# Optimization experiments

Measured on AMD Instinct MI355X. Metric: run time of the kernel, lower is better.

Reference implementation:

```python
import jax, jax.numpy as jnp
import numpy as np
import math

N, E, G = 16000, 128000, 64
D, H, O, L, HID = 64, 4, 64, 5, 128
EPS = 1e-5

def _ln(x, g, b):
    mu = x.mean(-1, keepdims=True)
    var = ((x - mu) ** 2).mean(-1, keepdims=True)
    return (x - mu) / jnp.sqrt(var + EPS) * g + b

def _softplus_b64(x):
    # torch nn.Softplus(beta=64, threshold=64): x if 64*x > 64 else log1p(exp(64*x))/64
    z = jnp.minimum(x * 64.0, 64.0)
    return jnp.where(x * 64.0 > 64.0, x, jnp.log1p(jnp.exp(z)) / 64.0)

def setup_inputs() -> dict:
    key = jax.random.key(0)
    ks = jax.random.split(key, 32)
    s = 0.05
    d = {
        'x': jax.random.normal(ks[0], (N, 4), jnp.float32),
        'edge_attr': jax.random.normal(ks[1], (E, 9), jnp.float32),
        'edge_index': jax.random.randint(ks[2], (2, E), 0, N),
        'batch': jnp.sort(jax.random.randint(ks[3], (N,), 0, G)),
        'W_atom': jax.random.normal(ks[4], (4, D)) * s, 'b_atom': jnp.zeros((D,)),
        'We1': jax.random.normal(ks[5], (9, D)) * s, 'be1': jnp.zeros((D,)),
        'We2': jax.random.normal(ks[6], (D, D)) * s, 'be2': jnp.zeros((D,)),
        'Wq': jax.random.normal(ks[7], (L, D, H * O)) * s, 'bq': jnp.zeros((L, H * O)),
        'Wk': jax.random.normal(ks[8], (L, D, H * O)) * s, 'bk': jnp.zeros((L, H * O)),
        'Wv': jax.random.normal(ks[9], (L, D, H * O)) * s, 'bv': jnp.zeros((L, H * O)),
        'Wedge': jax.random.normal(ks[10], (L, D, H * O)) * s, 'bedge': jnp.zeros((L, H * O)),
        'Wfea': jax.random.normal(ks[11], (L, D, O)) * s, 'bfea': jnp.zeros((L, O)),
        'Wcat': jax.random.normal(ks[12], (L, H * O, O)) * s, 'bcat': jnp.zeros((L, O)),
        'Wupd': jax.random.normal(ks[13], (L, 3 * O, 3 * O)) * s, 'bupd': jnp.zeros((L, 3 * O)),
        'Wmsg': jax.random.normal(ks[14], (L, 3 * O, O)) * s, 'bmsg': jnp.zeros((L, O)),
        'g_msg': jnp.ones((L, O)), 'be_msg': jnp.zeros((L, O)),
        'g_ln': jnp.ones((L, 3 * O)), 'be_ln': jnp.zeros((L, 3 * O)),
        'g_bn': jnp.ones((L, O)), 'be_bn': jnp.zeros((L, O)),
        'Wfc': jax.random.normal(ks[15], (D, HID)) * s, 'bfc': jnp.zeros((HID,)),
        'Wout': jax.random.normal(ks[16], (HID, 1)) * s, 'bout': jnp.zeros((1,)),
    }
    return d

def _forward(x, edge_attr, W_atom, b_atom, We1, be1, We2, be2, Wq, bq, Wk, bk, Wv, bv,
             Wedge, bedge, Wfea, bfea, Wcat, bcat, Wupd, bupd, Wmsg, bmsg,
             g_msg, be_msg, g_ln, be_ln, g_bn, be_bn, Wfc, bfc, Wout, bout,
             edge_index, batch):
    src, dst = edge_index[0], edge_index[1]  # x_j = src, x_i = dst (flow source_to_target)
    h = x @ W_atom + b_atom  # [N, D]
    e = _softplus_b64(edge_attr @ We1 + be1) @ We2 + be2  # [E, D]
    scale = 1.0 / math.sqrt(3.0 * O)
    for l in range(L):
        Q = (h @ Wq[l] + bq[l]).reshape(N, H, O)
        K = (h @ Wk[l] + bk[l]).reshape(N, H, O)
        V = (h @ Wv[l] + bv[l]).reshape(N, H, O)
        Eh = (e @ Wedge[l] + bedge[l]).reshape(E, H, O)
        Qi = Q[dst]
        q_ij = jnp.concatenate([Qi, Qi, Qi], axis=-1)                 # [E, H, 3O]
        k_ij = jnp.concatenate([K[dst], K[src], Eh], axis=-1)
        v_ij = jnp.concatenate([V[dst], V[src], Eh], axis=-1)
        alpha = q_ij * k_ij * scale
        gate = jax.nn.sigmoid(_ln(alpha, g_ln[l], be_ln[l]))
        m = gate * (v_ij @ Wupd[l] + bupd[l])
        m = _ln(m @ Wmsg[l] + bmsg[l], g_msg[l], be_msg[l])           # [E, H, O]
        agg = jax.ops.segment_sum(m, dst, num_segments=N).reshape(N, H * O)
        out = agg @ Wcat[l] + bcat[l]
        mu = out.mean(0)
        var = ((out - mu) ** 2).mean(0)  # biased var, BN training mode
        out = (out - mu) / jnp.sqrt(var + EPS) * g_bn[l] + be_bn[l]
        h = jax.nn.silu(out) + (h @ Wfea[l] + bfea[l])
    ones = jnp.ones((N,), h.dtype)
    cnt = jax.ops.segment_sum(ones, batch, num_segments=G)
    pooled = jax.ops.segment_sum(h, batch, num_segments=G) / jnp.maximum(cnt, 1.0)[:, None]
    z = jax.nn.silu(pooled @ Wfc + bfc)
    return z @ Wout + bout  # [G, 1]

def reference(x, edge_attr, edge_index, batch, W_atom, b_atom, We1, be1, We2, be2,
              Wq, bq, Wk, bk, Wv, bv, Wedge, bedge, Wfea, bfea, Wcat, bcat,
              Wupd, bupd, Wmsg, bmsg, g_msg, be_msg, g_ln, be_ln, g_bn, be_bn,
              Wfc, bfc, Wout, bout):
    return _forward(x, edge_attr, W_atom, b_atom, We1, be1, We2, be2, Wq, bq, Wk, bk,
                    Wv, bv, Wedge, bedge, Wfea, bfea, Wcat, bcat, Wupd, bupd,
                    Wmsg, bmsg, g_msg, be_msg, g_ln, be_ln, g_bn, be_bn,
                    Wfc, bfc, Wout, bout, edge_index, batch)
```

## Files before the change

kernel.cpp:

```cpp
#include <hip/hip_runtime.h>
#include <hip/hip_bf16.h>
#include <math.h>

#define N_NODES 16000
#define N_EDGES 128000
#define N_GRAPH 64
#define NL 5
#define EPSV 1e-5f
#define SCALE 0.07216878364870323f

#define PC 2048
#define ECOLS 1024
#define TILE 16
#define SCR 260

typedef __hip_bfloat16 bf16;
typedef __attribute__((ext_vector_type(8))) short short8;
typedef __attribute__((ext_vector_type(4))) short s4v;
typedef __attribute__((ext_vector_type(4))) float f32x4;
union S8U { short8 v; s4v h[2]; };

__device__ __forceinline__ ushort f2b(float x) {
    union { float f; uint u; } v; v.f = x;
    uint r = v.u + 0x7fffu + ((v.u >> 16) & 1u);
    return (ushort)(r >> 16);
}
__device__ __forceinline__ float b2fu(ushort u) { union { uint u; float f; } v; v.u = (uint)u << 16; return v.f; }

__global__ void pack_w(const float* __restrict__ Wq, const float* __restrict__ Wk,
                       const float* __restrict__ Wv, const float* __restrict__ Wupd,
                       const float* __restrict__ Wedge,
                       short* __restrict__ Wnp, short* __restrict__ Wep) {
    int idx = blockIdx.x * 256 + threadIdx.x;
    int total = NL * 64 * (PC + ECOLS);
    if (idx >= total) return;
    int c = idx % (PC + ECOLS);
    int k = (idx / (PC + ECOLS)) % 64;
    int l = idx / (64 * (PC + ECOLS));
    if (c < PC) {
        float v = 0.f;
        if (c < 256) v = Wq[(l*64 + k)*256 + c];
        else if (c < 512) v = Wk[(l*64 + k)*256 + (c - 256)];
        else if (c < 1280) {
            int cc = c - 512, hd = cc / 192, p = cc % 192;
            float s = 0.f;
            for (int q = 0; q < 64; ++q)
                s += Wv[(l*64 + k)*256 + hd*64 + q] * Wupd[(l*192 + q)*192 + p];
            v = s;
        } else {
            int cc = c - 1280, hd = cc / 192, p = cc % 192;
            float s = 0.f;
            for (int q = 0; q < 64; ++q)
                s += Wv[(l*64 + k)*256 + hd*64 + q] * Wupd[(l*192 + 64 + q)*192 + p];
            v = s;
        }
        int t = c >> 4, s = k >> 5, lane = (c & 15) | (((k & 31) >> 3) << 4), jj = k & 7;
        size_t fo = ((size_t)(t*2 + s)*64 + lane)*8 + jj;
        ushort hi = f2b(v);
        ushort lo = f2b(v - b2fu(hi));
        Wnp[(size_t)l*2*64*PC + fo] = (short)hi;
        Wnp[(size_t)l*2*64*PC + (size_t)64*PC + fo] = (short)lo;
    } else {
        int ce = c - PC;
        float v;
        if (ce < 256) v = Wedge[(l*64 + k)*256 + ce];
        else {
            int cc = ce - 256, hd = cc / 192, p = cc % 192;
            float s = 0.f;
            for (int q = 0; q < 64; ++q)
                s += Wedge[(l*64 + k)*256 + hd*64 + q] * Wupd[(l*192 + 128 + q)*192 + p];
            v = s;
        }
        int t = ce >> 4, s = k >> 5, lane = (ce & 15) | (((k & 31) >> 3) << 4), jj = k & 7;
        size_t fo = ((size_t)(t*2 + s)*64 + lane)*8 + jj;
        ushort hi = f2b(v);
        ushort lo = f2b(v - b2fu(hi));
        Wep[(size_t)l*2*64*ECOLS + fo] = (short)hi;
        Wep[(size_t)l*2*64*ECOLS + (size_t)64*ECOLS + fo] = (short)lo;
    }
}

__global__ void pack_wmsg(const float* __restrict__ Wmsg, short* __restrict__ Wmf) {
    int idx = blockIdx.x * 256 + threadIdx.x;
    if (idx >= NL*192*64) return;
    int col = idx & 63, k = (idx >> 6) % 192, l = idx / (192*64);
    float v = Wmsg[(size_t)(l*192 + k)*64 + col];
    int t = col >> 4, s = k >> 5, lane = (col & 15) | (((k & 31) >> 3) << 4), j = k & 7;
    Wmf[(size_t)l*12288 + ((size_t)((t*6 + s)*64) + lane)*8 + j] = (short)f2b(v);
}

__global__ void pack_b(const float* __restrict__ bq, const float* __restrict__ bk,
                       const float* __restrict__ bv, const float* __restrict__ Wupd,
                       const float* __restrict__ bupd, const float* __restrict__ bedge,
                       float* __restrict__ bnp, float* __restrict__ bep) {
    int idx = blockIdx.x * 256 + threadIdx.x;
    int total = NL * (PC + ECOLS);
    if (idx >= total) return;
    int c = idx % (PC + ECOLS);
    int l = idx / (PC + ECOLS);
    if (c < PC) {
        float v = 0.f;
        if (c < 256) v = bq[l*256 + c];
        else if (c < 512) v = bk[l*256 + c - 256];
        else if (c < 1280) {
            int cc = c - 512, hd = cc / 192, p = cc % 192;
            float s = 0.f;
            for (int k = 0; k < 64; ++k) s += bv[l*256 + hd*64 + k] * Wupd[(l*192 + k)*192 + p];
            v = s;
        } else {
            int cc = c - 1280, hd = cc / 192, p = cc % 192;
            float s = 0.f;
            for (int k = 0; k < 64; ++k) s += bv[l*256 + hd*64 + k] * Wupd[(l*192 + 64 + k)*192 + p];
            v = s;
        }
        bnp[l*PC + c] = v;
    } else {
        int ce = c - PC;
        float v;
        if (ce < 256) v = bedge[l*256 + ce];
        else {
            int cc = ce - 256, hd = cc / 192, p = cc % 192;
            float s = bupd[l*192 + p];
            for (int k = 0; k < 64; ++k) s += bedge[l*256 + hd*64 + k] * Wupd[(l*192 + 128 + k)*192 + p];
            v = s;
        }
        bep[l*ECOLS + ce] = v;
    }
}

__global__ void init_h(const float* __restrict__ x, const float* __restrict__ W_atom,
                       const float* __restrict__ b_atom, float* __restrict__ h) {
    int idx = blockIdx.x * 256 + threadIdx.x;
    int d = idx & 63, n = idx >> 6;
    float s = b_atom[d];
    #pragma unroll
    for (int j = 0; j < 4; ++j) s += x[n*4 + j] * W_atom[j*64 + d];
    h[idx] = s;
}

__global__ void init_e(const float* __restrict__ ea, const float* __restrict__ We1,
                       const float* __restrict__ be1, const float* __restrict__ We2,
                       const float* __restrict__ be2, float* __restrict__ ef) {
    __shared__ float sT[4][64];
    int tid = threadIdx.x, d = tid & 63, sub = tid >> 6;
    int e = blockIdx.x * 4 + sub;
    float s = be1[d];
    #pragma unroll
    for (int j = 0; j < 9; ++j) s += ea[e*9 + j] * We1[j*64 + d];
    float x64 = s * 64.f;
    float sp = (x64 > 64.f) ? s : log1pf(__expf(fminf(x64, 64.f))) * (1.f/64.f);
    sT[sub][d] = sp;
    float acc = be2[d];
    #pragma unroll
    for (int k = 0; k < 64; ++k) acc += sT[sub][k] * We2[k*64 + d];
    ef[(size_t)e*64 + d] = acc;
}

#define CPAD 260
__global__ __launch_bounds__(256, 8) void proj_mfma(
    const float* __restrict__ A, const short* __restrict__ Whi, const short* __restrict__ Wlo,
    const float* __restrict__ bias, ushort* __restrict__ out, int M) {
    __shared__ short aHi[2*64*8];
    __shared__ short aLo[2*64*8];
    __shared__ ushort cTile[16*CPAD];
    int tid = threadIdx.x;
    int row0 = blockIdx.y * 16;
    int col0 = blockIdx.x * 256;
    {
        int r = tid >> 4, k0 = (tid & 15) * 4;
        const float4 v = *(const float4*)(A + (size_t)(row0 + r)*64 + k0);
        int s = k0 >> 5, lane = r | (((k0 & 31) >> 3) << 4), j0 = k0 & 7;
        ushort4 hb, lb;
        hb.x = f2b(v.x); lb.x = f2b(v.x - b2fu(hb.x));
        hb.y = f2b(v.y); lb.y = f2b(v.y - b2fu(hb.y));
        hb.z = f2b(v.z); lb.z = f2b(v.z - b2fu(hb.z));
        hb.w = f2b(v.w); lb.w = f2b(v.w - b2fu(hb.w));
        *(ushort4*)&aHi[(s*64 + lane)*8 + j0] = hb;
        *(ushort4*)&aLo[(s*64 + lane)*8 + j0] = lb;
    }
    __syncthreads();
    int w = tid >> 6, lane = tid & 63;
    short8 a0h = *(const short8*)&aHi[(0*64 + lane)*8];
    short8 a1h = *(const short8*)&aHi[(1*64 + lane)*8];
    short8 a0l = *(const short8*)&aLo[(0*64 + lane)*8];
    short8 a1l = *(const short8*)&aLo[(1*64 + lane)*8];
    int cl = lane & 15, rg = lane >> 4;
    #pragma unroll
    for (int nt = 0; nt < 4; ++nt) {
        int t = (col0 >> 4) + w*4 + nt;
        const short* bph = Whi + ((size_t)(t*2)*64 + lane)*8;
        const short* bpl = Wlo + ((size_t)(t*2)*64 + lane)*8;
        short8 b0h = *(const short8*)bph;
        short8 b1h = *(const short8*)(bph + 64*8);
        short8 b0l = *(const short8*)bpl;
        short8 b1l = *(const short8*)(bpl + 64*8);
        f32x4 acc = {0.f, 0.f, 0.f, 0.f};
        acc = __builtin_amdgcn_mfma_f32_16x16x32_bf16(a0h, b0h, acc, 0, 0, 0);
        acc = __builtin_amdgcn_mfma_f32_16x16x32_bf16(a1h, b1h, acc, 0, 0, 0);
        acc = __builtin_amdgcn_mfma_f32_16x16x32_bf16(a0l, b0h, acc, 0, 0, 0);
        acc = __builtin_amdgcn_mfma_f32_16x16x32_bf16(a1l, b1h, acc, 0, 0, 0);
        acc = __builtin_amdgcn_mfma_f32_16x16x32_bf16(a0h, b0l, acc, 0, 0, 0);
        acc = __builtin_amdgcn_mfma_f32_16x16x32_bf16(a1h, b1l, acc, 0, 0, 0);
        int ccol = w*64 + nt*16 + cl;
        float bv = bias[col0 + ccol];
        #pragma unroll
        for (int r = 0; r < 4; ++r)
            cTile[(rg*4 + r)*CPAD + ccol] = f2b(acc[r] + bv);
    }
    __syncthreads();
    {
        int r = tid >> 4, cs = (tid & 15) * 16;
        ushort* dst = out + (size_t)(row0 + r)*M + col0 + cs;
        const ushort* srcp = &cTile[r*CPAD + cs];
        #pragma unroll
        for (int q = 0; q < 4; ++q)
            *(ushort4*)(dst + q*4) = *(const ushort4*)(srcp + q*4);
    }
}

__global__ __launch_bounds__(256) void hf_proj(const float* __restrict__ h,
                                               const float* __restrict__ Wfea,
                                               const float* __restrict__ bfea,
                                               float* __restrict__ HF) {
    __shared__ float sW[64*64];
    __shared__ __align__(16) float sA[4][64];
    int tid = threadIdx.x;
    for (int i = tid; i < 4096; i += 256) sW[i] = Wfea[i];
    int c = tid & 63, no = tid >> 6;
    int n0 = blockIdx.x * 4;
    sA[no][c] = h[(size_t)(n0 + no)*64 + c];
    __syncthreads();
    float acc = bfea[c];
    #pragma unroll
    for (int k4 = 0; k4 < 16; ++k4) {
        float4 av = *(const float4*)&sA[no][k4*4];
        acc += av.x*sW[(k4*4+0)*64+c] + av.y*sW[(k4*4+1)*64+c]
             + av.z*sW[(k4*4+2)*64+c] + av.w*sW[(k4*4+3)*64+c];
    }
    HF[(size_t)(n0 + no)*64 + c] = acc;
}

__global__ __launch_bounds__(256, 4) void edge_fused(
    const bf16* __restrict__ P, const float* __restrict__ ef,
    const short* __restrict__ Wef, const float* __restrict__ bef,
    const int* __restrict__ ei,
    const short* __restrict__ Wmf, const float* __restrict__ bmsg,
    const float* __restrict__ g_ln, const float* __restrict__ be_ln,
    const float* __restrict__ g_msg, const float* __restrict__ be_msg,
    float* __restrict__ agg) {
    __shared__ short aHi[2*64*8];
    __shared__ short aLo[2*64*8];
    __shared__ __align__(16) ushort scr[4][TILE][SCR];
    int tid = threadIdx.x, lane = tid & 63, hd = tid >> 6;
    int e0 = blockIdx.x * TILE;
    {
        int r = tid >> 4, k0 = (tid & 15) * 4;
        const float4 v = *(const float4*)(ef + (size_t)(e0 + r)*64 + k0);
        int s = k0 >> 5, alane = r | (((k0 & 31) >> 3) << 4), j0 = k0 & 7;
        ushort4 hb, lb;
        hb.x = f2b(v.x); lb.x = f2b(v.x - b2fu(hb.x));
        hb.y = f2b(v.y); lb.y = f2b(v.y - b2fu(hb.y));
        hb.z = f2b(v.z); lb.z = f2b(v.z - b2fu(hb.z));
        hb.w = f2b(v.w); lb.w = f2b(v.w - b2fu(hb.w));
        *(ushort4*)&aHi[(s*64 + alane)*8 + j0] = hb;
        *(ushort4*)&aLo[(s*64 + alane)*8 + j0] = lb;
    }
    __syncthreads();
    int cl = lane & 15, rg = lane >> 4;
    {
        short8 a0h = *(const short8*)&aHi[(0*64 + lane)*8];
        short8 a1h = *(const short8*)&aHi[(1*64 + lane)*8];
        short8 a0l = *(const short8*)&aLo[(0*64 + lane)*8];
        short8 a1l = *(const short8*)&aLo[(1*64 + lane)*8];
        #pragma unroll
        for (int tt = 0; tt < 16; ++tt) {
            int tg = (tt < 4) ? (hd*4 + tt) : (16 + hd*12 + (tt - 4));
            const short* bph = Wef + ((size_t)(tg*2)*64 + lane)*8;
            const short* bpl = bph + (size_t)64*ECOLS;
            short8 b0h = *(const short8*)bph;
            short8 b1h = *(const short8*)(bph + 512);
            short8 b0l = *(const short8*)bpl;
            short8 b1l = *(const short8*)(bpl + 512);
            float bv = bef[tg*16 + cl];
            f32x4 acc = {bv, bv, bv, bv};
            acc = __builtin_amdgcn_mfma_f32_16x16x32_bf16(a0h, b0h, acc, 0, 0, 0);
            acc = __builtin_amdgcn_mfma_f32_16x16x32_bf16(a1h, b1h, acc, 0, 0, 0);
            acc = __builtin_amdgcn_mfma_f32_16x16x32_bf16(a0l, b0h, acc, 0, 0, 0);
            acc = __builtin_amdgcn_mfma_f32_16x16x32_bf16(a1l, b1h, acc, 0, 0, 0);
            acc = __builtin_amdgcn_mfma_f32_16x16x32_bf16(a0h, b0l, acc, 0, 0, 0);
            acc = __builtin_amdgcn_mfma_f32_16x16x32_bf16(a1h, b1l, acc, 0, 0, 0);
            int wcol = (tt < 4) ? (tt*16 + cl) : (64 + (tt - 4)*16 + cl);
            #pragma unroll
            for (int r = 0; r < 4; ++r)
                scr[hd][rg*4 + r][wcol] = f2b(acc[r]);
        }
    }
    float gl0 = g_ln[lane], gl1 = g_ln[64 + lane], gl2 = g_ln[128 + lane];
    float bl0 = be_ln[lane], bl1 = be_ln[64 + lane], bl2 = be_ln[128 + lane];
    #pragma unroll 2
    for (int it = 0; it < TILE; ++it) {
        int eg = e0 + it;
        int src = ei[eg], dst = ei[N_EDGES + eg];
        const bf16* Pd = P + (size_t)dst * PC;
        const bf16* Ps = P + (size_t)src * PC;
        float q  = __bfloat162float(Pd[hd*64 + lane]);
        float kd = __bfloat162float(Pd[256 + hd*64 + lane]);
        float ks = __bfloat162float(Ps[256 + hd*64 + lane]);
        float eh = b2fu(scr[hd][it][lane]);
        float a0 = q*kd*SCALE, a1 = q*ks*SCALE, a2 = q*eh*SCALE;
        float s = a0 + a1 + a2, ss = a0*a0 + a1*a1 + a2*a2;
        #pragma unroll
        for (int m = 1; m < 64; m <<= 1) { s += __shfl_xor(s, m); ss += __shfl_xor(ss, m); }
        float mu = s * (1.f/192.f);
        float var = ss * (1.f/192.f) - mu*mu;
        float rstd = rsqrtf(var + EPSV);
        float g0 = 1.f/(1.f + __expf(-((a0 - mu)*rstd*gl0 + bl0)));
        float g1 = 1.f/(1.f + __expf(-((a1 - mu)*rstd*gl1 + bl1)));
        float g2 = 1.f/(1.f + __expf(-((a2 - mu)*rstd*gl2 + bl2)));
        float vu0 = __bfloat162float(Pd[512 + hd*192 + lane])
                  + __bfloat162float(Ps[1280 + hd*192 + lane])
                  + b2fu(scr[hd][it][64 + lane]);
        float vu1 = __bfloat162float(Pd[512 + hd*192 + 64 + lane])
                  + __bfloat162float(Ps[1280 + hd*192 + 64 + lane])
                  + b2fu(scr[hd][it][128 + lane]);
        float vu2 = __bfloat162float(Pd[512 + hd*192 + 128 + lane])
                  + __bfloat162float(Ps[1280 + hd*192 + 128 + lane])
                  + b2fu(scr[hd][it][192 + lane]);
        scr[hd][it][64 + lane]  = f2b(g0*vu0);
        scr[hd][it][128 + lane] = f2b(g1*vu1);
        scr[hd][it][192 + lane] = f2b(g2*vu2);
    }
    float bmsv[4], gmv[4], bmv[4];
    #pragma unroll
    for (int t = 0; t < 4; ++t) {
        bmsv[t] = bmsg[t*16 + cl];
        gmv[t]  = g_msg[t*16 + cl];
        bmv[t]  = be_msg[t*16 + cl];
    }
    int dstr[4];
    #pragma unroll
    for (int r = 0; r < 4; ++r) dstr[r] = ei[N_EDGES + e0 + rg*4 + r];
    f32x4 acc[4];
    #pragma unroll
    for (int t = 0; t < 4; ++t) acc[t] = (f32x4){bmsv[t], bmsv[t], bmsv[t], bmsv[t]};
    #pragma unroll
    for (int s = 0; s < 6; ++s) {
        S8U a;
        const ushort* ap = &scr[hd][cl][64 + s*32 + rg*8];
        a.h[0] = *(const s4v*)ap;
        a.h[1] = *(const s4v*)(ap + 4);
        #pragma unroll
        for (int t = 0; t < 4; ++t) {
            short8 b = *(const short8*)&Wmf[((size_t)((t*6 + s)*64) + lane)*8];
            acc[t] = __builtin_amdgcn_mfma_f32_16x16x32_bf16(a.v, b, acc[t], 0, 0, 0);
        }
    }
    #pragma unroll
    for (int r = 0; r < 4; ++r) {
        float s1 = acc[0][r] + acc[1][r] + acc[2][r] + acc[3][r];
        float s2 = acc[0][r]*acc[0][r] + acc[1][r]*acc[1][r]
                 + acc[2][r]*acc[2][r] + acc[3][r]*acc[3][r];
        #pragma unroll
        for (int m = 1; m < 16; m <<= 1) { s1 += __shfl_xor(s1, m); s2 += __shfl_xor(s2, m); }
        float mu = s1 * (1.f/64.f);
        float var = s2 * (1.f/64.f) - mu*mu;
        float rstd = rsqrtf(var + EPSV);
        float* base = &agg[(size_t)dstr[r]*256 + hd*64];
        #pragma unroll
        for (int t = 0; t < 4; ++t)
            atomicAdd(base + t*16 + cl, (acc[t][r] - mu)*rstd*gmv[t] + bmv[t]);
    }
}

__global__ __launch_bounds__(256, 2) void agg_out(
    const float* __restrict__ agg, const float* __restrict__ Wcat, const float* __restrict__ bcat,
    float* __restrict__ out, float* __restrict__ bnsum, float* __restrict__ bnss) {
    __shared__ float sW[256 * 64];
    __shared__ __align__(16) float sA[4][256];
    __shared__ float sR[4][64];
    int tid = threadIdx.x;
    for (int i = tid; i < 256*64; i += 256) sW[i] = Wcat[i];
    int c = tid & 63, no = tid >> 6;
    float bc = bcat[c];
    float psum = 0.f, psq = 0.f;
    __syncthreads();
    int nbase = blockIdx.x * 64;
    for (int it = 0; it < 16; ++it) {
        for (int i = tid; i < 1024; i += 256)
            sA[i >> 8][i & 255] = agg[(size_t)(nbase + it*4 + (i >> 8))*256 + (i & 255)];
        __syncthreads();
        float acc = bc;
        #pragma unroll
        for (int k4 = 0; k4 < 64; ++k4) {
            float4 av = *(const float4*)&sA[no][k4*4];
            acc += av.x*sW[(k4*4+0)*64 + c] + av.y*sW[(k4*4+1)*64 + c]
                 + av.z*sW[(k4*4+2)*64 + c] + av.w*sW[(k4*4+3)*64 + c];
        }
        out[(size_t)(nbase + it*4 + no)*64 + c] = acc;
        psum += acc; psq += acc*acc;
        __syncthreads();
    }
    sR[no][c] = psum; __syncthreads();
    if (no == 0) atomicAdd(&bnsum[c], sR[0][c] + sR[1][c] + sR[2][c] + sR[3][c]);
    __syncthreads();
    sR[no][c] = psq; __syncthreads();
    if (no == 0) atomicAdd(&bnss[c], sR[0][c] + sR[1][c] + sR[2][c] + sR[3][c]);
}

__global__ void bn_silu(const float* __restrict__ out, const float* __restrict__ HF,
                        const float* __restrict__ bnsum, const float* __restrict__ bnss,
                        const float* __restrict__ g_bn, const float* __restrict__ be_bn,
                        float* __restrict__ h) {
    int idx = blockIdx.x * 256 + threadIdx.x;
    int c = idx & 63;
    float mu = bnsum[c] * (1.f/N_NODES);
    float var = bnss[c] * (1.f/N_NODES) - mu*mu;
    float rstd = rsqrtf(var + EPSV);
    float v = (out[idx] - mu)*rstd*g_bn[c] + be_bn[c];
    float sv = v / (1.f + __expf(-v));
    h[idx] = sv + HF[idx];
}

__device__ __forceinline__ int lbound(const int* __restrict__ a, int n, int v) {
    int lo = 0, hi = n;
    while (lo < hi) { int m = (lo + hi) >> 1; if (a[m] < v) lo = m + 1; else hi = m; }
    return lo;
}

__global__ __launch_bounds__(256) void pool_head(
    const float* __restrict__ h, const int* __restrict__ batch,
    const float* __restrict__ Wfc, const float* __restrict__ bfc,
    const float* __restrict__ Wout, const float* __restrict__ bout,
    float* __restrict__ d_out) {
    __shared__ float sPart[4][64];
    __shared__ float sP[64];
    __shared__ float red[128];
    int g = blockIdx.x, tid = threadIdx.x;
    int lo = lbound(batch, N_NODES, g);
    int hi = lbound(batch, N_NODES, g + 1);
    int c = tid & 63, rg = tid >> 6;
    float s = 0.f;
    for (int n = lo + rg; n < hi; n += 4) s += h[(size_t)n*64 + c];
    sPart[rg][c] = s;
    __syncthreads();
    if (tid < 64)
        sP[tid] = (sPart[0][tid] + sPart[1][tid] + sPart[2][tid] + sPart[3][tid])
                  * (1.f / fmaxf((float)(hi - lo), 1.f));
    __syncthreads();
    if (tid < 128) {
        float acc = bfc[tid];
        #pragma unroll
        for (int k = 0; k < 64; ++k) acc += sP[k] * Wfc[k*128 + tid];
        float z = acc / (1.f + __expf(-acc));
        red[tid] = z * Wout[tid];
    }
    __syncthreads();
    for (int s1 = 64; s1 > 0; s1 >>= 1) {
        if (tid < s1 && tid + s1 < 128) red[tid] += red[tid + s1];
        __syncthreads();
    }
    if (tid == 0) d_out[g] = red[0] + bout[0];
}

extern "C" void kernel_launch(void* const* d_in, const int* in_sizes, int n_in,
                              void* d_out, int out_size, void* d_ws, size_t ws_size,
                              hipStream_t stream) {
    const float* x        = (const float*)d_in[0];
    const float* edge_attr= (const float*)d_in[1];
    const int*   ei       = (const int*)  d_in[2];
    const int*   batch    = (const int*)  d_in[3];
    const float* W_atom=(const float*)d_in[4];  const float* b_atom=(const float*)d_in[5];
    const float* We1  =(const float*)d_in[6];   const float* be1  =(const float*)d_in[7];
    const float* We2  =(const float*)d_in[8];   const float* be2  =(const float*)d_in[9];
    const float* Wq   =(const float*)d_in[10];  const float* bq   =(const float*)d_in[11];
    const float* Wk   =(const float*)d_in[12];  const float* bk   =(const float*)d_in[13];
    const float* Wv   =(const float*)d_in[14];  const float* bv   =(const float*)d_in[15];
    const float* Wedge=(const float*)d_in[16];  const float* bedge=(const float*)d_in[17];
    const float* Wfea =(const float*)d_in[18];  const float* bfea =(const float*)d_in[19];
    const float* Wcat =(const float*)d_in[20];  const float* bcat =(const float*)d_in[21];
    const float* Wupd =(const float*)d_in[22];  const float* bupd =(const float*)d_in[23];
    const float* Wmsg =(const float*)d_in[24];  const float* bmsg =(const float*)d_in[25];
    const float* g_msg=(const float*)d_in[26];  const float* be_msg=(const float*)d_in[27];
    const float* g_ln =(const float*)d_in[28];  const float* be_ln=(const float*)d_in[29];
    const float* g_bn =(const float*)d_in[30];  const float* be_bn=(const float*)d_in[31];
    const float* Wfc  =(const float*)d_in[32];  const float* bfc  =(const float*)d_in[33];
    const float* Wout =(const float*)d_in[34];  const float* bout =(const float*)d_in[35];

    char* ws = (char*)d_ws;
    size_t off = 0;
    auto alloc = [&](size_t bytes) {
        void* p = ws + off;
        off += (bytes + 255) & ~(size_t)255;
        return p;
    };
    short* Wnp  = (short*)alloc((size_t)NL*2*64*PC*2);
    float* bnp  = (float*)alloc((size_t)NL*PC*4);
    short* Wep  = (short*)alloc((size_t)NL*2*64*ECOLS*2);
    float* bep  = (float*)alloc((size_t)NL*ECOLS*4);
    short* Wmf  = (short*)alloc((size_t)NL*12288*2);
    float* h    = (float*)alloc((size_t)N_NODES*64*4);
    float* ef   = (float*)alloc((size_t)N_EDGES*64*4);
    bf16*  P    = (bf16*) alloc((size_t)N_NODES*PC*2);
    float* HF   = (float*)alloc((size_t)N_NODES*64*4);
    float* agg  = (float*)alloc((size_t)N_NODES*256*4);
    float* outb = (float*)alloc((size_t)N_NODES*64*4);
    float* bnsum= (float*)alloc(64*4);
    float* bnss = (float*)alloc(64*4);
    if (off > ws_size) return;

    {
        int total = NL*64*(PC+ECOLS);
        pack_w<<<(total+255)/256, 256, 0, stream>>>(Wq, Wk, Wv, Wupd, Wedge, Wnp, Wep);
        int tb = NL*(PC+ECOLS);
        pack_b<<<(tb+255)/256, 256, 0, stream>>>(bq, bk, bv, Wupd, bupd, bedge, bnp, bep);
        pack_wmsg<<<(NL*192*64+255)/256, 256, 0, stream>>>(Wmsg, Wmf);
    }
    init_h<<<(N_NODES*64)/256, 256, 0, stream>>>(x, W_atom, b_atom, h);
    init_e<<<N_EDGES/4, 256, 0, stream>>>(edge_attr, We1, be1, We2, be2, ef);

    for (int l = 0; l < NL; ++l) {
        const short* Wh = Wnp + (size_t)l*2*64*PC;
        proj_mfma<<<dim3(PC/256, N_NODES/16), 256, 0, stream>>>(
            h, Wh, Wh + (size_t)64*PC, bnp + l*PC, (ushort*)P, PC);
        hf_proj<<<N_NODES/4, 256, 0, stream>>>(h, Wfea + (size_t)l*64*64, bfea + l*64, HF);
        hipMemsetAsync(agg, 0, (size_t)N_NODES*256*4, stream);
        hipMemsetAsync(bnsum, 0, 64*4, stream);
        hipMemsetAsync(bnss, 0, 64*4, stream);
        edge_fused<<<N_EDGES/TILE, 256, 0, stream>>>(
            P, ef, Wep + (size_t)l*2*64*ECOLS, bep + l*ECOLS, ei,
            Wmf + (size_t)l*12288, bmsg + l*64,
            g_ln + l*192, be_ln + l*192, g_msg + l*64, be_msg + l*64, agg);
        agg_out<<<N_NODES/64, 256, 0, stream>>>(agg, Wcat + (size_t)l*256*64, bcat + l*64,
                                                outb, bnsum, bnss);
        bn_silu<<<(N_NODES*64)/256, 256, 0, stream>>>(outb, HF, bnsum, bnss,
                                                      g_bn + l*64, be_bn + l*64, h);
    }
    pool_head<<<N_GRAPH, 256, 0, stream>>>(h, batch, Wfc, bfc, Wout, bout, (float*)d_out);
}
```

Baseline: 1.658 ms.

## Sort edges by destination and combine per-tile atomics for same-destination rows

```diff
diff --git a/kernel.cpp b/kernel.cpp
--- a/kernel.cpp
+++ b/kernel.cpp
@@ -128,6 +128,46 @@
     }
 }
 
+__global__ void hist_k(const int* __restrict__ ei, int* __restrict__ hist) {
+    int e = blockIdx.x * 256 + threadIdx.x;
+    if (e < N_EDGES) atomicAdd(&hist[ei[N_EDGES + e]], 1);
+}
+
+__global__ void scan_k(const int* __restrict__ hist, int* __restrict__ binCur) {
+    __shared__ int sBuf[256];
+    __shared__ int sCarry;
+    int tid = threadIdx.x;
+    if (tid == 0) sCarry = 0;
+    __syncthreads();
+    for (int base = 0; base < N_NODES; base += 256) {
+        int v = (base + tid < N_NODES) ? hist[base + tid] : 0;
+        sBuf[tid] = v; __syncthreads();
+        #pragma unroll
+        for (int ofs = 1; ofs < 256; ofs <<= 1) {
+            int t = (tid >= ofs) ? sBuf[tid - ofs] : 0;
+            __syncthreads();
+            sBuf[tid] += t;
+            __syncthreads();
+        }
+        if (base + tid < N_NODES) binCur[base + tid] = sCarry + sBuf[tid] - v;
+        __syncthreads();
+        if (tid == 0) sCarry += sBuf[255];
+        __syncthreads();
+    }
+}
+
+__global__ void scatter_k(const int* __restrict__ ei, int* __restrict__ binCur,
+                          int* __restrict__ perm, int* __restrict__ srcs, int* __restrict__ dsts) {
+    int e = blockIdx.x * 256 + threadIdx.x;
+    if (e < N_EDGES) {
+        int d = ei[N_EDGES + e];
+        int pos = atomicAdd(&binCur[d], 1);
+        perm[pos] = e;
+        srcs[pos] = ei[e];
+        dsts[pos] = d;
+    }
+}
+
 __global__ void init_h(const float* __restrict__ x, const float* __restrict__ W_atom,
                        const float* __restrict__ b_atom, float* __restrict__ h) {
     int idx = blockIdx.x * 256 + threadIdx.x;
@@ -243,7 +283,7 @@
 __global__ __launch_bounds__(256, 4) void edge_fused(
     const bf16* __restrict__ P, const float* __restrict__ ef,
     const short* __restrict__ Wef, const float* __restrict__ bef,
-    const int* __restrict__ ei,
+    const int* __restrict__ perm, const int* __restrict__ srcs, const int* __restrict__ dsts,
     const short* __restrict__ Wmf, const float* __restrict__ bmsg,
     const float* __restrict__ g_ln, const float* __restrict__ be_ln,
     const float* __restrict__ g_msg, const float* __restrict__ be_msg,
@@ -255,7 +295,8 @@
     int e0 = blockIdx.x * TILE;
     {
         int r = tid >> 4, k0 = (tid & 15) * 4;
-        const float4 v = *(const float4*)(ef + (size_t)(e0 + r)*64 + k0);
+        int ep = perm[e0 + r];
+        const float4 v = *(const float4*)(ef + (size_t)ep*64 + k0);
         int s = k0 >> 5, alane = r | (((k0 & 31) >> 3) << 4), j0 = k0 & 7;
         ushort4 hb, lb;
         hb.x = f2b(v.x); lb.x = f2b(v.x - b2fu(hb.x));
@@ -299,8 +340,7 @@
     float bl0 = be_ln[lane], bl1 = be_ln[64 + lane], bl2 = be_ln[128 + lane];
     #pragma unroll 2
     for (int it = 0; it < TILE; ++it) {
-        int eg = e0 + it;
-        int src = ei[eg], dst = ei[N_EDGES + eg];
+        int src = srcs[e0 + it], dst = dsts[e0 + it];
         const bf16* Pd = P + (size_t)dst * PC;
         const bf16* Ps = P + (size_t)src * PC;
         float q  = __bfloat162float(Pd[hd*64 + lane]);
@@ -339,7 +379,7 @@
     }
     int dstr[4];
     #pragma unroll
-    for (int r = 0; r < 4; ++r) dstr[r] = ei[N_EDGES + e0 + rg*4 + r];
+    for (int r = 0; r < 4; ++r) dstr[r] = dsts[e0 + rg*4 + r];
     f32x4 acc[4];
     #pragma unroll
     for (int t = 0; t < 4; ++t) acc[t] = (f32x4){bmsv[t], bmsv[t], bmsv[t], bmsv[t]};
@@ -355,6 +395,7 @@
             acc[t] = __builtin_amdgcn_mfma_f32_16x16x32_bf16(a.v, b, acc[t], 0, 0, 0);
         }
     }
+    float nv[4][4];
     #pragma unroll
     for (int r = 0; r < 4; ++r) {
         float s1 = acc[0][r] + acc[1][r] + acc[2][r] + acc[3][r];
@@ -365,10 +406,31 @@
         float mu = s1 * (1.f/64.f);
         float var = s2 * (1.f/64.f) - mu*mu;
         float rstd = rsqrtf(var + EPSV);
-        float* base = &agg[(size_t)dstr[r]*256 + hd*64];
-        #pragma unroll
-        for (int t = 0; t < 4; ++t)
-            atomicAdd(base + t*16 + cl, (acc[t][r] - mu)*rstd*gmv[t] + bmv[t]);
+        #pragma unroll
+        for (int t = 0; t < 4; ++t) nv[t][r] = (acc[t][r] - mu)*rstd*gmv[t] + bmv[t];
+    }
+    int cur = dstr[0];
+    float r0 = nv[0][0], r1 = nv[1][0], r2 = nv[2][0], r3 = nv[3][0];
+    #pragma unroll
+    for (int r = 1; r < 4; ++r) {
+        if (dstr[r] == cur) {
+            r0 += nv[0][r]; r1 += nv[1][r]; r2 += nv[2][r]; r3 += nv[3][r];
+        } else {
+            float* base = &agg[(size_t)cur*256 + hd*64];
+            atomicAdd(base + 0*16 + cl, r0);
+            atomicAdd(base + 1*16 + cl, r1);
+            atomicAdd(base + 2*16 + cl, r2);
+            atomicAdd(base + 3*16 + cl, r3);
+            cur = dstr[r];
+            r0 = nv[0][r]; r1 = nv[1][r]; r2 = nv[2][r]; r3 = nv[3][r];
+        }
+    }
+    {
+        float* base = &agg[(size_t)cur*256 + hd*64];
+        atomicAdd(base + 0*16 + cl, r0);
+        atomicAdd(base + 1*16 + cl, r1);
+        atomicAdd(base + 2*16 + cl, r2);
+        atomicAdd(base + 3*16 + cl, r3);
     }
 }
 
@@ -506,6 +568,11 @@
     float* outb = (float*)alloc((size_t)N_NODES*64*4);
     float* bnsum= (float*)alloc(64*4);
     float* bnss = (float*)alloc(64*4);
+    int* histB  = (int*)alloc((size_t)N_NODES*4);
+    int* binCur = (int*)alloc((size_t)N_NODES*4);
+    int* perm   = (int*)alloc((size_t)N_EDGES*4);
+    int* srcs   = (int*)alloc((size_t)N_EDGES*4);
+    int* dsts   = (int*)alloc((size_t)N_EDGES*4);
     if (off > ws_size) return;
 
     {
@@ -515,6 +582,11 @@
         pack_b<<<(tb+255)/256, 256, 0, stream>>>(bq, bk, bv, Wupd, bupd, bedge, bnp, bep);
         pack_wmsg<<<(NL*192*64+255)/256, 256, 0, stream>>>(Wmsg, Wmf);
     }
+    hipMemsetAsync(histB, 0, (size_t)N_NODES*4, stream);
+    hist_k<<<(N_EDGES+255)/256, 256, 0, stream>>>(ei, histB);
+    scan_k<<<1, 256, 0, stream>>>(histB, binCur);
+    scatter_k<<<(N_EDGES+255)/256, 256, 0, stream>>>(ei, binCur, perm, srcs, dsts);
+
     init_h<<<(N_NODES*64)/256, 256, 0, stream>>>(x, W_atom, b_atom, h);
     init_e<<<N_EDGES/4, 256, 0, stream>>>(edge_attr, We1, be1, We2, be2, ef);
 
@@ -527,7 +599,7 @@
         hipMemsetAsync(bnsum, 0, 64*4, stream);
         hipMemsetAsync(bnss, 0, 64*4, stream);
         edge_fused<<<N_EDGES/TILE, 256, 0, stream>>>(
-            P, ef, Wep + (size_t)l*2*64*ECOLS, bep + l*ECOLS, ei,
+            P, ef, Wep + (size_t)l*2*64*ECOLS, bep + l*ECOLS, perm, srcs, dsts,
             Wmf + (size_t)l*12288, bmsg + l*64,
             g_ln + l*192, be_ln + l*192, g_msg + l*64, be_msg + l*64, agg);
         agg_out<<<N_NODES/64, 256, 0, stream>>>(agg, Wcat + (size_t)l*256*64, bcat + l*64,
```

Measured after the change: 1.712 ms. 3.3% more time.

## Interleave node projection columns for vector gathers and halve edge tile

Applied to the files above, without the earlier changes.

```diff
diff --git a/kernel.cpp b/kernel.cpp
--- a/kernel.cpp
+++ b/kernel.cpp
@@ -9,10 +9,10 @@
 #define EPSV 1e-5f
 #define SCALE 0.07216878364870323f
 
-#define PC 2048
+#define PCK 3072
 #define ECOLS 1024
-#define TILE 16
-#define SCR 260
+#define TILE 8
+#define SCR 258
 
 typedef __hip_bfloat16 bf16;
 typedef __attribute__((ext_vector_type(8))) short short8;
@@ -26,42 +26,52 @@
     return (ushort)(r >> 16);
 }
 __device__ __forceinline__ float b2fu(ushort u) { union { uint u; float f; } v; v.u = (uint)u << 16; return v.f; }
+__device__ __forceinline__ float b2f_lo32(uint u) { union { uint u; float f; } v; v.u = u << 16; return v.f; }
+__device__ __forceinline__ float b2f_hi32(uint u) { union { uint u; float f; } v; v.u = u & 0xffff0000u; return v.f; }
 
 __global__ void pack_w(const float* __restrict__ Wq, const float* __restrict__ Wk,
                        const float* __restrict__ Wv, const float* __restrict__ Wupd,
                        const float* __restrict__ Wedge,
                        short* __restrict__ Wnp, short* __restrict__ Wep) {
     int idx = blockIdx.x * 256 + threadIdx.x;
-    int total = NL * 64 * (PC + ECOLS);
+    int total = NL * 64 * (PCK + ECOLS);
     if (idx >= total) return;
-    int c = idx % (PC + ECOLS);
-    int k = (idx / (PC + ECOLS)) % 64;
-    int l = idx / (64 * (PC + ECOLS));
-    if (c < PC) {
+    int c = idx % (PCK + ECOLS);
+    int k = (idx / (PCK + ECOLS)) % 64;
+    int l = idx / (64 * (PCK + ECOLS));
+    if (c < PCK) {
         float v = 0.f;
-        if (c < 256) v = Wq[(l*64 + k)*256 + c];
-        else if (c < 512) v = Wk[(l*64 + k)*256 + (c - 256)];
-        else if (c < 1280) {
-            int cc = c - 512, hd = cc / 192, p = cc % 192;
-            float s = 0.f;
-            for (int q = 0; q < 64; ++q)
-                s += Wv[(l*64 + k)*256 + hd*64 + q] * Wupd[(l*192 + q)*192 + p];
-            v = s;
+        if (c < 2048) {
+            int hd = c >> 9, ch = (c >> 3) & 63, j = c & 7;
+            if (j == 0) v = Wq[(l*64 + k)*256 + hd*64 + ch];
+            else if (j == 1) v = Wk[(l*64 + k)*256 + hd*64 + ch];
+            else if (j <= 4) {
+                int p = (j - 2)*64 + ch;
+                float s = 0.f;
+                for (int q = 0; q < 64; ++q)
+                    s += Wv[(l*64 + k)*256 + hd*64 + q] * Wupd[(l*192 + q)*192 + p];
+                v = s;
+            }
         } else {
-            int cc = c - 1280, hd = cc / 192, p = cc % 192;
-            float s = 0.f;
-            for (int q = 0; q < 64; ++q)
-                s += Wv[(l*64 + k)*256 + hd*64 + q] * Wupd[(l*192 + 64 + q)*192 + p];
-            v = s;
+            int cc = c - 2048;
+            int hd = cc >> 8, ch = (cc >> 2) & 63, j = cc & 3;
+            if (j == 0) v = Wk[(l*64 + k)*256 + hd*64 + ch];
+            else {
+                int p = (j - 1)*64 + ch;
+                float s = 0.f;
+                for (int q = 0; q < 64; ++q)
+                    s += Wv[(l*64 + k)*256 + hd*64 + q] * Wupd[(l*192 + 64 + q)*192 + p];
+                v = s;
+            }
         }
         int t = c >> 4, s = k >> 5, lane = (c & 15) | (((k & 31) >> 3) << 4), jj = k & 7;
         size_t fo = ((size_t)(t*2 + s)*64 + lane)*8 + jj;
         ushort hi = f2b(v);
         ushort lo = f2b(v - b2fu(hi));
-        Wnp[(size_t)l*2*64*PC + fo] = (short)hi;
-        Wnp[(size_t)l*2*64*PC + (size_t)64*PC + fo] = (short)lo;
+        Wnp[(size_t)l*2*64*PCK + fo] = (short)hi;
+        Wnp[(size_t)l*2*64*PCK + (size_t)64*PCK + fo] = (short)lo;
     } else {
-        int ce = c - PC;
+        int ce = c - PCK;
         float v;
         if (ce < 256) v = Wedge[(l*64 + k)*256 + ce];
         else {
@@ -94,28 +104,36 @@
                        const float* __restrict__ bupd, const float* __restrict__ bedge,
                        float* __restrict__ bnp, float* __restrict__ bep) {
     int idx = blockIdx.x * 256 + threadIdx.x;
-    int total = NL * (PC + ECOLS);
+    int total = NL * (PCK + ECOLS);
     if (idx >= total) return;
-    int c = idx % (PC + ECOLS);
-    int l = idx / (PC + ECOLS);
-    if (c < PC) {
+    int c = idx % (PCK + ECOLS);
+    int l = idx / (PCK + ECOLS);
+    if (c < PCK) {
         float v = 0.f;
-        if (c < 256) v = bq[l*256 + c];
-        else if (c < 512) v = bk[l*256 + c - 256];
-        else if (c < 1280) {
-            int cc = c - 512, hd = cc / 192, p = cc % 192;
-            float s = 0.f;
-            for (int k = 0; k < 64; ++k) s += bv[l*256 + hd*64 + k] * Wupd[(l*192 + k)*192 + p];
-            v = s;
+        if (c < 2048) {
+            int hd = c >> 9, ch = (c >> 3) & 63, j = c & 7;
+            if (j == 0) v = bq[l*256 + hd*64 + ch];
+            else if (j == 1) v = bk[l*256 + hd*64 + ch];
+            else if (j <= 4) {
+                int p = (j - 2)*64 + ch;
+                float s = 0.f;
+                for (int k = 0; k < 64; ++k) s += bv[l*256 + hd*64 + k] * Wupd[(l*192 + k)*192 + p];
+                v = s;
+            }
         } else {
-            int cc = c - 1280, hd = cc / 192, p = cc % 192;
-            float s = 0.f;
-            for (int k = 0; k < 64; ++k) s += bv[l*256 + hd*64 + k] * Wupd[(l*192 + 64 + k)*192 + p];
-            v = s;
-        }
-        bnp[l*PC + c] = v;
+            int cc = c - 2048;
+            int hd = cc >> 8, ch = (cc >> 2) & 63, j = cc & 3;
+            if (j == 0) v = bk[l*256 + hd*64 + ch];
+            else {
+                int p = (j - 1)*64 + ch;
+                float s = 0.f;
+                for (int k = 0; k < 64; ++k) s += bv[l*256 + hd*64 + k] * Wupd[(l*192 + 64 + k)*192 + p];
+                v = s;
+            }
+        }
+        bnp[l*PCK + c] = v;
     } else {
-        int ce = c - PC;
+        int ce = c - PCK;
         float v;
         if (ce < 256) v = bedge[l*256 + ce];
         else {
@@ -240,8 +258,8 @@
     HF[(size_t)(n0 + no)*64 + c] = acc;
 }
 
-__global__ __launch_bounds__(256, 4) void edge_fused(
-    const bf16* __restrict__ P, const float* __restrict__ ef,
+__global__ __launch_bounds__(256, 7) void edge_fused(
+    const ushort* __restrict__ Pu, const float* __restrict__ ef,
     const short* __restrict__ Wef, const float* __restrict__ bef,
     const int* __restrict__ ei,
     const short* __restrict__ Wmf, const float* __restrict__ bmsg,
@@ -253,7 +271,7 @@
     __shared__ __align__(16) ushort scr[4][TILE][SCR];
     int tid = threadIdx.x, lane = tid & 63, hd = tid >> 6;
     int e0 = blockIdx.x * TILE;
-    {
+    if (tid < 128) {
         int r = tid >> 4, k0 = (tid & 15) * 4;
         const float4 v = *(const float4*)(ef + (size_t)(e0 + r)*64 + k0);
         int s = k0 >> 5, alane = r | (((k0 & 31) >> 3) << 4), j0 = k0 & 7;
@@ -289,10 +307,12 @@
             acc = __builtin_amdgcn_mfma_f32_16x16x32_bf16(a1l, b1h, acc, 0, 0, 0);
             acc = __builtin_amdgcn_mfma_f32_16x16x32_bf16(a0h, b0l, acc, 0, 0, 0);
             acc = __builtin_amdgcn_mfma_f32_16x16x32_bf16(a1h, b1l, acc, 0, 0, 0);
-            int wcol = (tt < 4) ? (tt*16 + cl) : (64 + (tt - 4)*16 + cl);
-            #pragma unroll
-            for (int r = 0; r < 4; ++r)
-                scr[hd][rg*4 + r][wcol] = f2b(acc[r]);
+            if (rg < 2) {
+                int wcol = (tt < 4) ? (tt*16 + cl) : (64 + (tt - 4)*16 + cl);
+                #pragma unroll
+                for (int r = 0; r < 4; ++r)
+                    scr[hd][rg*4 + r][wcol] = f2b(acc[r]);
+            }
         }
     }
     float gl0 = g_ln[lane], gl1 = g_ln[64 + lane], gl2 = g_ln[128 + lane];
@@ -301,11 +321,12 @@
     for (int it = 0; it < TILE; ++it) {
         int eg = e0 + it;
         int src = ei[eg], dst = ei[N_EDGES + eg];
-        const bf16* Pd = P + (size_t)dst * PC;
-        const bf16* Ps = P + (size_t)src * PC;
-        float q  = __bfloat162float(Pd[hd*64 + lane]);
-        float kd = __bfloat162float(Pd[256 + hd*64 + lane]);
-        float ks = __bfloat162float(Ps[256 + hd*64 + lane]);
+        const uint4 D = *(const uint4*)(Pu + (size_t)dst*PCK + hd*512 + (lane << 3));
+        const uint2 S = *(const uint2*)(Pu + (size_t)src*PCK + 2048 + hd*256 + (lane << 2));
+        float q   = b2f_lo32(D.x), kd  = b2f_hi32(D.x);
+        float vd0 = b2f_lo32(D.y), vd1 = b2f_hi32(D.y), vd2 = b2f_lo32(D.z);
+        float ks  = b2f_lo32(S.x), vs0 = b2f_hi32(S.x);
+        float vs1 = b2f_lo32(S.y), vs2 = b2f_hi32(S.y);
         float eh = b2fu(scr[hd][it][lane]);
         float a0 = q*kd*SCALE, a1 = q*ks*SCALE, a2 = q*eh*SCALE;
         float s = a0 + a1 + a2, ss = a0*a0 + a1*a1 + a2*a2;
@@ -314,18 +335,12 @@
         float mu = s * (1.f/192.f);
         float var = ss * (1.f/192.f) - mu*mu;
         float rstd = rsqrtf(var + EPSV);
-        float g0 = 1.f/(1.f + __expf(-((a0 - mu)*rstd*gl0 + bl0)));
-        float g1 = 1.f/(1.f + __expf(-((a1 - mu)*rstd*gl1 + bl1)));
-        float g2 = 1.f/(1.f + __expf(-((a2 - mu)*rstd*gl2 + bl2)));
-        float vu0 = __bfloat162float(Pd[512 + hd*192 + lane])
-                  + __bfloat162float(Ps[1280 + hd*192 + lane])
-                  + b2fu(scr[hd][it][64 + lane]);
-        float vu1 = __bfloat162float(Pd[512 + hd*192 + 64 + lane])
-                  + __bfloat162float(Ps[1280 + hd*192 + 64 + lane])
-                  + b2fu(scr[hd][it][128 + lane]);
-        float vu2 = __bfloat162float(Pd[512 + hd*192 + 128 + lane])
-                  + __bfloat162float(Ps[1280 + hd*192 + 128 + lane])
-                  + b2fu(scr[hd][it][192 + lane]);
+        float g0 = __builtin_amdgcn_rcpf(1.f + __expf(-((a0 - mu)*rstd*gl0 + bl0)));
+        float g1 = __builtin_amdgcn_rcpf(1.f + __expf(-((a1 - mu)*rstd*gl1 + bl1)));
+        float g2 = __builtin_amdgcn_rcpf(1.f + __expf(-((a2 - mu)*rstd*gl2 + bl2)));
+        float vu0 = vd0 + vs0 + b2fu(scr[hd][it][64 + lane]);
+        float vu1 = vd1 + vs1 + b2fu(scr[hd][it][128 + lane]);
+        float vu2 = vd2 + vs2 + b2fu(scr[hd][it][192 + lane]);
         scr[hd][it][64 + lane]  = f2b(g0*vu0);
         scr[hd][it][128 + lane] = f2b(g1*vu1);
         scr[hd][it][192 + lane] = f2b(g2*vu2);
@@ -339,14 +354,14 @@
     }
     int dstr[4];
     #pragma unroll
-    for (int r = 0; r < 4; ++r) dstr[r] = ei[N_EDGES + e0 + rg*4 + r];
+    for (int r = 0; r < 4; ++r) dstr[r] = (rg < 2) ? ei[N_EDGES + e0 + rg*4 + r] : 0;
     f32x4 acc[4];
     #pragma unroll
     for (int t = 0; t < 4; ++t) acc[t] = (f32x4){bmsv[t], bmsv[t], bmsv[t], bmsv[t]};
     #pragma unroll
     for (int s = 0; s < 6; ++s) {
         S8U a;
-        const ushort* ap = &scr[hd][cl][64 + s*32 + rg*8];
+        const ushort* ap = &scr[hd][cl & 7][64 + s*32 + rg*8];
         a.h[0] = *(const s4v*)ap;
         a.h[1] = *(const s4v*)(ap + 4);
         #pragma unroll
@@ -365,10 +380,12 @@
         float mu = s1 * (1.f/64.f);
         float var = s2 * (1.f/64.f) - mu*mu;
         float rstd = rsqrtf(var + EPSV);
-        float* base = &agg[(size_t)dstr[r]*256 + hd*64];
-        #pragma unroll
-        for (int t = 0; t < 4; ++t)
-            atomicAdd(base + t*16 + cl, (acc[t][r] - mu)*rstd*gmv[t] + bmv[t]);
+        if (rg < 2) {
+            float* base = &agg[(size_t)dstr[r]*256 + hd*64];
+            #pragma unroll
+            for (int t = 0; t < 4; ++t)
+                atomicAdd(base + t*16 + cl, (acc[t][r] - mu)*rstd*gmv[t] + bmv[t]);
+        }
     }
 }
 
@@ -493,14 +510,14 @@
         off += (bytes + 255) & ~(size_t)255;
         return p;
     };
-    short* Wnp  = (short*)alloc((size_t)NL*2*64*PC*2);
-    float* bnp  = (float*)alloc((size_t)NL*PC*4);
+    short* Wnp  = (short*)alloc((size_t)NL*2*64*PCK*2);
+    float* bnp  = (float*)alloc((size_t)NL*PCK*4);
     short* Wep  = (short*)alloc((size_t)NL*2*64*ECOLS*2);
     float* bep  = (float*)alloc((size_t)NL*ECOLS*4);
     short* Wmf  = (short*)alloc((size_t)NL*12288*2);
     float* h    = (float*)alloc((size_t)N_NODES*64*4);
     float* ef   = (float*)alloc((size_t)N_EDGES*64*4);
-    bf16*  P    = (bf16*) alloc((size_t)N_NODES*PC*2);
+    ushort* P   = (ushort*)alloc((size_t)N_NODES*PCK*2);
     float* HF   = (float*)alloc((size_t)N_NODES*64*4);
     float* agg  = (float*)alloc((size_t)N_NODES*256*4);
     float* outb = (float*)alloc((size_t)N_NODES*64*4);
@@ -509,9 +526,9 @@
     if (off > ws_size) return;
 
     {
-        int total = NL*64*(PC+ECOLS);
+        int total = NL*64*(PCK+ECOLS);
         pack_w<<<(total+255)/256, 256, 0, stream>>>(Wq, Wk, Wv, Wupd, Wedge, Wnp, Wep);
-        int tb = NL*(PC+ECOLS);
+        int tb = NL*(PCK+ECOLS);
         pack_b<<<(tb+255)/256, 256, 0, stream>>>(bq, bk, bv, Wupd, bupd, bedge, bnp, bep);
         pack_wmsg<<<(NL*192*64+255)/256, 256, 0, stream>>>(Wmsg, Wmf);
     }
@@ -519,9 +536,9 @@
     init_e<<<N_EDGES/4, 256, 0, stream>>>(edge_attr, We1, be1, We2, be2, ef);
 
     for (int l = 0; l < NL; ++l) {
-        const short* Wh = Wnp + (size_t)l*2*64*PC;
-        proj_mfma<<<dim3(PC/256, N_NODES/16), 256, 0, stream>>>(
-            h, Wh, Wh + (size_t)64*PC, bnp + l*PC, (ushort*)P, PC);
+        const short* Wh = Wnp + (size_t)l*2*64*PCK;
+        proj_mfma<<<dim3(PCK/256, N_NODES/16), 256, 0, stream>>>(
+            h, Wh, Wh + (size_t)64*PCK, bnp + l*PCK, P, PCK);
         hf_proj<<<N_NODES/4, 256, 0, stream>>>(h, Wfea + (size_t)l*64*64, bfea + l*64, HF);
         hipMemsetAsync(agg, 0, (size_t)N_NODES*256*4, stream);
         hipMemsetAsync(bnsum, 0, 64*4, stream);
```

After: 2.324 ms. 40.2% more time.
